# Kernel tuning notes

Measured on AMD Instinct MI355X. Metric: run time of the kernel, lower is better.

## Reference

```python
import jax, jax.numpy as jnp
import numpy as np
import math

N, T, IN = 2048, 128, 64
H = 256           # hidden_dim
NH, HD = 2, 128   # num_heads, head_dim (NH*HD == H)
C = 30            # rows of R
OUT = 1           # output_dim


def setup_inputs() -> dict:
    key = jax.random.key(0)
    ks = jax.random.split(key, 24)
    s = lambda k, shape, sc: (jax.random.normal(k, shape, dtype=jnp.float32) * sc)
    g = 1.0 / math.sqrt(H)
    d = {}
    d['x'] = s(ks[0], (N, T, IN), 1.0)
    # GRU layer 0 (input IN -> H); gate order r,z,n as in torch
    d['W_ih0'] = s(ks[1], (3 * H, IN), g)
    d['W_hh0'] = s(ks[2], (3 * H, H), g)
    d['b_ih0'] = s(ks[3], (3 * H,), g)
    d['b_hh0'] = s(ks[4], (3 * H,), g)
    # GRU layer 1 (H -> H)
    d['W_ih1'] = s(ks[5], (3 * H, H), g)
    d['W_hh1'] = s(ks[6], (3 * H, H), g)
    d['b_ih1'] = s(ks[7], (3 * H,), g)
    d['b_hh1'] = s(ks[8], (3 * H,), g)
    # per-head Q/K/V linears, stacked over heads: [NH, H, HD] (+ bias [NH, HD])
    d['Wq'] = s(ks[9], (NH, H, HD), g)
    d['bq'] = s(ks[10], (NH, HD), g)
    d['Wk'] = s(ks[11], (NH, H, HD), g)
    d['bk'] = s(ks[12], (NH, HD), g)
    d['Wv'] = s(ks[13], (NH, H, HD), g)
    d['bv'] = s(ks[14], (NH, HD), g)
    # fixed random memory R [C, H]
    d['R'] = s(ks[15], (C, H), 1.0)
    # gate, mlp1, mlp2
    d['W_gate'] = s(ks[16], (1, H), g)
    d['b_gate'] = s(ks[17], (1,), g)
    d['W1'] = s(ks[18], (H, H), g)
    d['b1'] = s(ks[19], (H,), g)
    d['W2'] = s(ks[20], (OUT, H), g)
    d['b2'] = s(ks[21], (OUT,), g)
    return d


def _gru_layer(xs, Wih, Whh, bih, bhh):
    # xs: [N, T, D_in] -> [N, T, H]; PyTorch GRU equations, gate order r,z,n
    xW = jnp.einsum('nti,gi->ntg', xs, Wih) + bih  # [N,T,3H] precompute input path
    h0 = jnp.zeros((xs.shape[0], H), xs.dtype)

    def step(h, xt):
        gh = h @ Whh.T + bhh                      # [N,3H]
        r = jax.nn.sigmoid(xt[:, :H] + gh[:, :H])
        z = jax.nn.sigmoid(xt[:, H:2 * H] + gh[:, H:2 * H])
        n = jnp.tanh(xt[:, 2 * H:] + r * gh[:, 2 * H:])
        hn = (1.0 - z) * n + z * h
        return hn, hn

    _, ys = jax.lax.scan(step, h0, jnp.swapaxes(xW, 0, 1))
    return jnp.swapaxes(ys, 0, 1)


def _mha(q, k, v, Wq, bq, Wk, bk, Wv, bv):
    # q:[Lq,H] k,v:[Lk,H]; vectorized over heads (replaces the per-head Python loop)
    qh = jnp.einsum('ld,ndh->nlh', q, Wq) + bq[:, None, :]
    kh = jnp.einsum('ld,ndh->nlh', k, Wk) + bk[:, None, :]
    vh = jnp.einsum('ld,ndh->nlh', v, Wv) + bv[:, None, :]
    p = jax.nn.softmax(jnp.einsum('nqh,nkh->nqk', qh, kh) / math.sqrt(HD), axis=-1)
    o = jnp.einsum('nqk,nkh->nqh', p, vh)
    # concat heads along last dim, head order preserved
    return jnp.swapaxes(o, 0, 1).reshape(q.shape[0], NH * HD)


def reference(x, W_ih0, W_hh0, b_ih0, b_hh0, W_ih1, W_hh1, b_ih1, b_hh1,
              Wq, bq, Wk, bk, Wv, bv, R, W_gate, b_gate, W1, b1, W2, b2):
    out = _gru_layer(x, W_ih0, W_hh0, b_ih0, b_hh0)
    out = _gru_layer(out, W_ih1, W_hh1, b_ih1, b_hh1)
    S = out[:, -1, :]                               # [N, H]
    B = _mha(R, S, S, Wq, bq, Wk, bk, Wv, bv)       # [C, H]
    S_prime = _mha(S, B, B, Wq, bq, Wk, bk, Wv, bv) # [N, H]
    alpha = jax.nn.sigmoid(S @ W_gate.T + b_gate)   # [N,1], broadcasts like expand_as
    S_mix = alpha * S_prime + (1.0 - alpha) * S
    h = jax.nn.relu(S_mix @ W1.T + b1)              # dropout = identity (eval mode)
    S_mix = h + S_mix
    y = (S_mix @ W2.T + b2).reshape(-1)             # [N*OUT]
    return (y - y.mean()) / (y.std(ddof=1) + 1e-8)  # torch.std is unbiased (ddof=1)
```

## Files before the change

kernel.cpp:

```cpp
#include <hip/hip_runtime.h>
#include <hip/hip_bf16.h>


#define HH  256
#define TT  128
#define INP 64
#define KH  8

typedef float f32x4 __attribute__((ext_vector_type(4)));
typedef short bf16x8 __attribute__((ext_vector_type(8)));
typedef unsigned long long u64;

#define MFMA(A,B,C) __builtin_amdgcn_mfma_f32_16x16x32_bf16((A),(B),(C),0,0,0)

__device__ __forceinline__ float bf2f(unsigned short s) {
    unsigned u = ((unsigned)s) << 16;
    float f; __builtin_memcpy(&f, &u, 4); return f;
}
__device__ __forceinline__ unsigned short f2bf(float f) {
    unsigned u; __builtin_memcpy(&u, &f, 4);
    unsigned r = (u + 0x7FFFu + ((u >> 16) & 1u)) >> 16;
    return (unsigned short)r;
}

__device__ __forceinline__ float sigm(float x) {
    float t = __builtin_amdgcn_exp2f(x * -1.442695040889f);
    return __builtin_amdgcn_rcpf(1.f + t);
}
__device__ __forceinline__ float tanhfast(float x) {
    float xc = fminf(fmaxf(x, -15.f), 15.f);
    float t = __builtin_amdgcn_exp2f(xc * 2.885390081778f);
    return (t - 1.f) * __builtin_amdgcn_rcpf(t + 1.f);
}


__global__ void pack_w(const float* __restrict__ Whh, const float* __restrict__ Wih,
                       int Kin, int Kw, unsigned short* __restrict__ FBhi,
                       unsigned short* __restrict__ FBlo, int total)
{
    int idx = blockIdx.x * 256 + threadIdx.x;
    if (idx >= total) return;
    int n = idx / Kw, k = idx - n * Kw;
    float v = (k < 256) ? Whh[n * 256 + k] : Wih[n * Kin + (k - 256)];
    int dst = (n >> 4) * (Kw * 16) + (k >> 5) * 512 + ((k >> 3) & 3) * 128 + (n & 15) * 8 + (k & 7);
    unsigned short h = f2bf(v);
    FBhi[dst] = h;
    FBlo[dst] = f2bf(v - bf2f(h));
}

__global__ void pack_x(const float* __restrict__ x, unsigned short* __restrict__ FXhi)
{
    int idx = blockIdx.x * 256 + threadIdx.x;
    int k = idx & 63;
    int t = (idx >> 6) & 127;
    int m = idx >> 13;
    int dst = t * 131072 + (m >> 4) * 1024 + (k >> 5) * 512 + ((k >> 3) & 3) * 128 + (m & 15) * 8 + (k & 7);
    FXhi[dst] = f2bf(x[idx]);
}

template<int NKC, int STRIDE>
__device__ __forceinline__ void stage_Bs(const unsigned short* __restrict__ Bhi,
                                         const unsigned short* __restrict__ Blo,
                                         short* __restrict__ sB, int ntb, int tid)
{
    const int Kw16 = NKC * 512;
#pragma unroll 1
    for (int t = tid; t < 3 * NKC * 64; t += STRIDE) {
        const int g = t / (NKC * 64);
        const int r = t - g * (NKC * 64);
        *(bf16x8*)(sB + g * Kw16 + r * 8) =
            *(const bf16x8*)(Bhi + (g * 16 + ntb) * Kw16 + r * 8);
        *(bf16x8*)(sB + 3 * Kw16 + g * Kw16 + r * 8) =
            *(const bf16x8*)(Blo + (g * 16 + ntb) * Kw16 + r * 8);
    }
}

template<int NKC, bool LAY>
__device__ __forceinline__ void gru_core(
    const unsigned short* Ah_h, const unsigned short* Al_h,
    const unsigned short* Ah_x, const unsigned short* Al_x,
    const short* __restrict__ sB, int mt0, int lane,
    f32x4 (&ar)[2], f32x4 (&az)[2], f32x4 (&anh)[2], f32x4 (&anx)[2])
{
    const int Kw16 = NKC * 512;
    const int xs = LAY ? 4096 : 1024;
    const int lo8 = lane * 8;
    const short* sH = sB + lo8;
    const short* sL = sB + 3 * Kw16 + lo8;

    bf16x8 A[4][2][2];
    bf16x8 B[3][3][2];

    auto ldA = [&](int kc, bf16x8 (&Ax)[2][2]) {
        if (kc < KH) {
#pragma unroll
            for (int mt = 0; mt < 2; ++mt) {
                Ax[mt][0] = *(const bf16x8*)(Ah_h + (mt0 + mt) * 4096 + kc * 512 + lo8);
                Ax[mt][1] = *(const bf16x8*)(Al_h + (mt0 + mt) * 4096 + kc * 512 + lo8);
            }
        } else {
#pragma unroll
            for (int mt = 0; mt < 2; ++mt) {
                Ax[mt][0] = *(const bf16x8*)(Ah_x + (mt0 + mt) * xs + (kc - KH) * 512 + lo8);
                if (LAY)
                    Ax[mt][1] = *(const bf16x8*)(Al_x + (mt0 + mt) * xs + (kc - KH) * 512 + lo8);
            }
        }
    };
    auto ldB = [&](int kc, bf16x8 (&Bx)[3][2]) {
#pragma unroll
        for (int g = 0; g < 3; ++g) {
            Bx[g][0] = *(const bf16x8*)(sH + g * Kw16 + kc * 512);
            Bx[g][1] = *(const bf16x8*)(sL + g * Kw16 + kc * 512);
        }
    };

    ldA(0, A[0]);
    if (NKC > 1) ldA(1, A[1]);
    if (NKC > 2) ldA(2, A[2]);
    ldB(0, B[0]);
    if (NKC > 1) ldB(1, B[1]);
#pragma unroll
    for (int kc = 0; kc < NKC; ++kc) {
        if (kc + 3 < NKC) ldA(kc + 3, A[(kc + 3) & 3]);
        if (kc + 2 < NKC) ldB(kc + 2, B[(kc + 2) % 3]);
        const bool hp = (kc < KH);
        const bool a3 = LAY || hp;
        bf16x8 (&cA)[2][2] = A[kc & 3];
        bf16x8 (&cB)[3][2] = B[kc % 3];
#pragma unroll
        for (int mt = 0; mt < 2; ++mt) {
            ar[mt] = MFMA(cA[mt][0], cB[0][0], ar[mt]);
            ar[mt] = MFMA(cA[mt][0], cB[0][1], ar[mt]);
            if (a3) ar[mt] = MFMA(cA[mt][1], cB[0][0], ar[mt]);
            az[mt] = MFMA(cA[mt][0], cB[1][0], az[mt]);
            az[mt] = MFMA(cA[mt][0], cB[1][1], az[mt]);
            if (a3) az[mt] = MFMA(cA[mt][1], cB[1][0], az[mt]);
            if (hp) {
                anh[mt] = MFMA(cA[mt][0], cB[2][0], anh[mt]);
                anh[mt] = MFMA(cA[mt][0], cB[2][1], anh[mt]);
                if (a3) anh[mt] = MFMA(cA[mt][1], cB[2][0], anh[mt]);
            } else {
                anx[mt] = MFMA(cA[mt][0], cB[2][0], anx[mt]);
                anx[mt] = MFMA(cA[mt][0], cB[2][1], anx[mt]);
                if (a3) anx[mt] = MFMA(cA[mt][1], cB[2][0], anx[mt]);
            }
        }
    }
}

__device__ __forceinline__ void xcd_bar(unsigned* cnt, unsigned need)
{
    __syncthreads();
    if (threadIdx.x == 0) {
        __hip_atomic_fetch_add(cnt, 1u, __ATOMIC_RELAXED, __HIP_MEMORY_SCOPE_AGENT);
        while (__hip_atomic_load(cnt, __ATOMIC_RELAXED, __HIP_MEMORY_SCOPE_AGENT) < need)
            __builtin_amdgcn_s_sleep(1);
    }
    __syncthreads();
    asm volatile("buffer_inv\n\ts_waitcnt vmcnt(0)" ::: "memory");
}

__global__ __launch_bounds__(512, 2) void gru_scan(
    unsigned short* H0hiA, unsigned short* H0loA,
    unsigned short* H0hiB, unsigned short* H0loB,
    unsigned short* H1hiA, unsigned short* H1loA,
    unsigned short* H1hiB, unsigned short* H1loB,
    const unsigned short* __restrict__ FXhi,
    const unsigned short* __restrict__ FB0hi, const unsigned short* __restrict__ FB0lo,
    const unsigned short* __restrict__ FB1hi, const unsigned short* __restrict__ FB1lo,
    const float* __restrict__ bih0, const float* __restrict__ bhh0,
    const float* __restrict__ bih1, const float* __restrict__ bhh1,
    float* __restrict__ S1f, unsigned* bar, int* xslot)
{
    const int tid = threadIdx.x;
    int xcc;
    asm volatile("s_getreg_b32 %0, hwreg(HW_REG_XCC_ID)" : "=s"(xcc));
    xcc &= 7;
    __shared__ int sSlot;
    if (tid == 0) sSlot = atomicAdd(&xslot[xcc], 1) & 31;
    __syncthreads();
    const int slot = sSlot;
    const int mb2 = slot >> 4;
    const int cb = slot & 15;
    const int w = tid >> 6, lane = tid & 63;
    const int lay = w >> 2, wl = w & 3;
    const int l15 = lane & 15, q = lane >> 4;
    const int mt0 = xcc * 16 + mb2 * 8 + wl * 2;
    const int ntb = cb;
    unsigned* cnt = bar + (xcc * 2 + mb2) * 32;

    __shared__ __align__(16) short sB[79872];
    short* sB1 = sB;
    short* sB0 = sB + 49152;
    stage_Bs<16, 512>(FB1hi, FB1lo, sB1, cb, tid);
    stage_Bs<10, 512>(FB0hi, FB0lo, sB0, cb, tid);
    __syncthreads();

    const float* bih = lay ? bih1 : bih0;
    const float* bhh = lay ? bhh1 : bhh0;
    const int c = (ntb << 4) + l15;
    const float brb = bih[c] + bhh[c];
    const float bzb = bih[256 + c] + bhh[256 + c];
    const float bni = bih[512 + c];
    const float bnh = bhh[512 + c];
    const int cfr = (c >> 5) * 512 + ((c >> 3) & 3) * 128 + (c & 7);

    float hreg[2][4];
#pragma unroll
    for (int mt = 0; mt < 2; ++mt)
#pragma unroll
        for (int rg = 0; rg < 4; ++rg) hreg[mt][rg] = 0.f;

    for (int i = 0; i <= TT; ++i) {
        const int p = i & 1;
        const unsigned short* H0r_hi = p ? H0hiB : H0hiA;
        const unsigned short* H0r_lo = p ? H0loB : H0loA;
        unsigned short*       H0w_hi = p ? H0hiA : H0hiB;
        unsigned short*       H0w_lo = p ? H0loA : H0loB;
        const unsigned short* H1r_hi = p ? H1hiB : H1hiA;
        const unsigned short* H1r_lo = p ? H1loB : H1loA;
        unsigned short*       H1w_hi = p ? H1hiA : H1hiB;
        unsigned short*       H1w_lo = p ? H1loA : H1loB;

        const bool active = lay ? (i >= 1) : (i < TT);
        if (active) {
            f32x4 ar[2], az[2], anh[2], anx[2];
#pragma unroll
            for (int j = 0; j < 2; ++j) {
                ar[j] = (f32x4){0.f,0.f,0.f,0.f}; az[j] = (f32x4){0.f,0.f,0.f,0.f};
                anh[j] = (f32x4){0.f,0.f,0.f,0.f}; anx[j] = (f32x4){0.f,0.f,0.f,0.f};
            }
            if (lay) {
                gru_core<16, true>(H1r_hi, H1r_lo, H0r_hi, H0r_lo, sB1,
                                   mt0, lane, ar, az, anh, anx);
            } else {
                gru_core<10, false>(H0r_hi, H0r_lo, FXhi + i * 131072,
                                    (const unsigned short*)0, sB0,
                                    mt0, lane, ar, az, anh, anx);
            }

            unsigned short* Whi = lay ? H1w_hi : H0w_hi;
            unsigned short* Wlo = lay ? H1w_lo : H0w_lo;

#pragma unroll
            for (int mt = 0; mt < 2; ++mt) {
                const int mtg = mt0 + mt;
                const int fbase = mtg * 4096 + cfr;
#pragma unroll
                for (int rg = 0; rg < 4; ++rg) {
                    const int mi = q * 4 + rg;
                    const int fidx = fbase + mi * 8;
                    const float rr = sigm(ar[mt][rg] + brb);
                    const float zz = sigm(az[mt][rg] + bzb);
                    const float nn = tanhfast(anx[mt][rg] + bni + rr * (anh[mt][rg] + bnh));
                    const float hn = (1.f - zz) * nn + zz * hreg[mt][rg];
                    const unsigned short hb = f2bf(hn);
                    const unsigned short lb = f2bf(hn - bf2f(hb));
                    Whi[fidx] = hb;
                    Wlo[fidx] = lb;
                    hreg[mt][rg] = bf2f(hb) + bf2f(lb);
                    if (lay && i == TT) S1f[(mtg * 16 + mi) * 256 + c] = hn;
                }
            }
        }
        if (i < TT) xcd_bar(cnt, 16u * (unsigned)(i + 1));
    }
}


__global__ __launch_bounds__(256) void proj_gemm(const float* __restrict__ S,
    const float* __restrict__ Wk, const float* __restrict__ bk,
    const float* __restrict__ Wv, const float* __restrict__ bv,
    const float* __restrict__ Wq, const float* __restrict__ bq,
    float* __restrict__ ok, float* __restrict__ ov, float* __restrict__ oq)
{
    __shared__ float sT[256][65];
    const int bid = blockIdx.x;
    const int p = bid >> 6;
    const int h = (bid >> 5) & 1;
    const int l0 = (bid & 31) * 64;
    const int tid = threadIdx.x;
    const float* W = (p == 0) ? Wk : ((p == 1) ? Wv : Wq);
    const float* b = (p == 0) ? bk : ((p == 1) ? bv : bq);
    float* o = (p == 0) ? ok : ((p == 1) ? ov : oq);

    for (int e = tid; e < 64 * 256; e += 256) {
        int k = e & 255, l = e >> 8;
        sT[k][l] = S[(l0 + l) * 256 + k];
    }
    __syncthreads();

    const int dg = tid & 15, lg = tid >> 4;
    const int d0 = dg * 8;
    const float* Wp = W + h * 32768 + d0;
    float acc[4][8];
#pragma unroll
    for (int i = 0; i < 4; ++i)
#pragma unroll
        for (int j = 0; j < 8; ++j) acc[i][j] = 0.f;

    for (int k = 0; k < 256; ++k) {
        f32x4 sv = *(const f32x4*)&sT[k][lg * 4];
        f32x4 w0 = *(const f32x4*)(Wp + k * 128);
        f32x4 w1 = *(const f32x4*)(Wp + k * 128 + 4);
#pragma unroll
        for (int i = 0; i < 4; ++i) {
#pragma unroll
            for (int j = 0; j < 4; ++j) {
                acc[i][j]     += sv[i] * w0[j];
                acc[i][4 + j] += sv[i] * w1[j];
            }
        }
    }
#pragma unroll
    for (int i = 0; i < 4; ++i) {
        float* op = o + (h * 2048 + l0 + lg * 4 + i) * 128 + d0;
#pragma unroll
        for (int j = 0; j < 8; ++j) op[j] = acc[i][j] + b[h * 128 + d0 + j];
    }
}

__global__ void proj3_kernel(const float* __restrict__ A, int M,
    const float* __restrict__ Wk, const float* __restrict__ bk,
    const float* __restrict__ Wv, const float* __restrict__ bv,
    float* __restrict__ ok, float* __restrict__ ov)
{
    int idx = blockIdx.x * 256 + threadIdx.x;
    if (idx >= 2 * 2 * M * 128) return;
    int d = idx & 127;
    int rest = idx >> 7;
    int l = rest % M;
    int ph = rest / M;
    int h = ph & 1, p = ph >> 1;
    const float* W = (p == 0) ? Wk : Wv;
    const float* b = (p == 0) ? bk : bv;
    float* o = (p == 0) ? ok : ov;
    float accv = b[h * 128 + d];
    const float* a = A + l * 256;
    const float* wp = W + h * (256 * 128) + d;
    for (int j = 0; j < 256; ++j) accv += a[j] * wp[j * 128];
    o[(h * M + l) * 128 + d] = accv;
}

__global__ void projR_kernel(const float* __restrict__ R,
    const float* __restrict__ Wq, const float* __restrict__ bq,
    float* __restrict__ oq)
{
    int idx = blockIdx.x * 256 + threadIdx.x;
    if (idx >= 2 * 30 * 128) return;
    int d = idx & 127;
    int rest = idx >> 7;
    int l = rest % 30;
    int h = rest / 30;
    float a = bq[h * 128 + d];
    const float* r = R + l * 256;
    const float* wp = Wq + h * 32768 + d;
    for (int j = 0; j < 256; ++j) a += r[j] * wp[j * 128];
    oq[(h * 30 + l) * 128 + d] = a;
}

__global__ void scores1_kernel(const float* __restrict__ qhR, const float* __restrict__ kh,
                               float* __restrict__ s1)
{
    int idx = blockIdx.x * 256 + threadIdx.x;
    if (idx >= 2 * 30 * 2048) return;
    int k = idx & 2047;
    int rest = idx >> 11;
    int i = rest % 30;
    int h = rest / 30;
    const f32x4* qp = (const f32x4*)(qhR + (h * 30 + i) * 128);
    const f32x4* kp = (const f32x4*)(kh + (h * 2048 + k) * 128);
    float acc = 0.f;
    for (int dd = 0; dd < 32; ++dd) {
        f32x4 a = qp[dd], b = kp[dd];
        acc += a[0] * b[0] + a[1] * b[1] + a[2] * b[2] + a[3] * b[3];
    }
    s1[idx] = acc * 0.08838834764831845f;
}

__global__ void softmax1_kernel(float* __restrict__ s1)
{
    __shared__ float red[256];
    float* p = s1 + blockIdx.x * 2048;
    int tid = threadIdx.x;
    float mx = -1e30f;
    for (int k = tid; k < 2048; k += 256) mx = fmaxf(mx, p[k]);
    red[tid] = mx; __syncthreads();
    for (int s = 128; s > 0; s >>= 1) { if (tid < s) red[tid] = fmaxf(red[tid], red[tid + s]); __syncthreads(); }
    mx = red[0]; __syncthreads();
    float sum = 0.f;
    for (int k = tid; k < 2048; k += 256) { float e = expf(p[k] - mx); p[k] = e; sum += e; }
    red[tid] = sum; __syncthreads();
    for (int s = 128; s > 0; s >>= 1) { if (tid < s) red[tid] += red[tid + s]; __syncthreads(); }
    float inv = 1.f / red[0];
    for (int k = tid; k < 2048; k += 256) p[k] *= inv;
}

__global__ void o1_kernel(const float* __restrict__ p1, const float* __restrict__ vh,
                          float* __restrict__ Bm)
{
    int bid = blockIdx.x;
    int row = bid >> 4;
    int ks = bid & 15;
    int h = row / 30;
    int i = row % 30;
    int d = threadIdx.x;
    const float* pp = p1 + row * 2048 + ks * 128;
    const float* vp = vh + (h * 2048 + ks * 128) * 128 + d;
    float acc = 0.f;
    for (int k = 0; k < 128; ++k) acc += pp[k] * vp[k * 128];
    atomicAdd(&Bm[i * 256 + h * 128 + d], acc);
}

__global__ __launch_bounds__(256) void attn2_kernel(
    const float* __restrict__ qh2, const float* __restrict__ kh2, const float* __restrict__ vh2,
    const float* __restrict__ S, const float* __restrict__ Wg,
    const float* __restrict__ bg, float* __restrict__ Smix)
{
    __shared__ float ks[2 * 30 * 129];
    __shared__ float qred[256];
    __shared__ float ps[64];
    int l = blockIdx.x;
    int tid = threadIdx.x;
    for (int idx = tid; idx < 2 * 30 * 128; idx += 256) {
        int hh = idx / 3840; int rem = idx - hh * 3840;
        int j = rem >> 7; int d = rem & 127;
        ks[(hh * 30 + j) * 129 + d] = kh2[idx];
    }
    int h = tid >> 7, d = tid & 127;
    qred[tid] = qh2[(h * 2048 + l) * 128 + d];
    __syncthreads();
    int w = tid >> 6, lane = tid & 63;
    if (w < 2 && lane < 32) {
        float sc = -1e30f;
        if (lane < 30) {
            const float* qp = qred + w * 128;
            float a = 0.f;
            for (int dd = 0; dd < 128; ++dd) a += qp[dd] * ks[(w * 30 + lane) * 129 + dd];
            sc = a * 0.08838834764831845f;
        }
        float mx = sc;
        for (int m = 16; m > 0; m >>= 1) mx = fmaxf(mx, __shfl_xor(mx, m, 32));
        float e = (lane < 30) ? expf(sc - mx) : 0.f;
        float sm = e;
        for (int m = 16; m > 0; m >>= 1) sm += __shfl_xor(sm, m, 32);
        ps[w * 32 + lane] = e / sm;
    }
    __syncthreads();
    float o = 0.f;
    const float* vp = vh2 + h * 3840 + d;
    for (int j = 0; j < 30; ++j) o += ps[h * 32 + j] * vp[j * 128];
    float sl = S[l * 256 + tid];
    qred[tid] = sl * Wg[tid];
    __syncthreads();
    for (int s = 128; s > 0; s >>= 1) { if (tid < s) qred[tid] += qred[tid + s]; __syncthreads(); }
    float alpha = 1.f / (1.f + expf(-(qred[0] + bg[0])));
    Smix[l * 256 + tid] = alpha * o + (1.f - alpha) * sl;
}

__global__ void w1t_kernel(const float* __restrict__ W1, float* __restrict__ W1T)
{
    int idx = blockIdx.x * 256 + threadIdx.x;
    int j = idx & 255, c = idx >> 8;
    W1T[j * 256 + c] = W1[c * 256 + j];
}

__global__ void mlp_kernel(const float* __restrict__ Smix, const float* __restrict__ W1T,
                           const float* __restrict__ b1, float* __restrict__ S2)
{
    int idx = blockIdx.x * 256 + threadIdx.x;
    int c = idx & 255; int l = idx >> 8;
    const float* a = Smix + l * 256;
    float acc = b1[c];
    for (int j = 0; j < 256; ++j) acc += a[j] * W1T[j * 256 + c];
    float v = fmaxf(acc, 0.f);
    S2[idx] = v + a[c];
}

__global__ void y_kernel(const float* __restrict__ S2, const float* __restrict__ W2,
                         const float* __restrict__ b2, float* __restrict__ y)
{
    __shared__ float red[256];
    int l = blockIdx.x; int tid = threadIdx.x;
    red[tid] = S2[l * 256 + tid] * W2[tid];
    __syncthreads();
    for (int s = 128; s > 0; s >>= 1) { if (tid < s) red[tid] += red[tid + s]; __syncthreads(); }
    if (tid == 0) y[l] = red[0] + b2[0];
}

__global__ void norm_kernel(const float* __restrict__ y, float* __restrict__ out)
{
    __shared__ float r1[1024], r2[1024];
    int tid = threadIdx.x;
    float s1v = 0.f, s2v = 0.f;
    for (int idx = tid; idx < 2048; idx += 1024) { float v = y[idx]; s1v += v; s2v += v * v; }
    r1[tid] = s1v; r2[tid] = s2v; __syncthreads();
    for (int s = 512; s > 0; s >>= 1) {
        if (tid < s) { r1[tid] += r1[tid + s]; r2[tid] += r2[tid + s]; }
        __syncthreads();
    }
    float mean = r1[0] / 2048.f;
    float var = fmaxf((r2[0] - 2048.f * mean * mean) / 2047.f, 0.f);
    float inv = 1.f / (sqrtf(var) + 1e-8f);
    for (int idx = tid; idx < 2048; idx += 1024)
        out[idx] = (y[idx] - mean) * inv;
}

extern "C" void kernel_launch(void* const* d_in, const int* in_sizes, int n_in,
                              void* d_out, int out_size, void* d_ws, size_t ws_size,
                              hipStream_t stream)
{
    const float* x    = (const float*)d_in[0];
    const float* Wih0 = (const float*)d_in[1];
    const float* Whh0 = (const float*)d_in[2];
    const float* bih0 = (const float*)d_in[3];
    const float* bhh0 = (const float*)d_in[4];
    const float* Wih1 = (const float*)d_in[5];
    const float* Whh1 = (const float*)d_in[6];
    const float* bih1 = (const float*)d_in[7];
    const float* bhh1 = (const float*)d_in[8];
    const float* Wq   = (const float*)d_in[9];
    const float* bq   = (const float*)d_in[10];
    const float* Wk   = (const float*)d_in[11];
    const float* bk   = (const float*)d_in[12];
    const float* Wv   = (const float*)d_in[13];
    const float* bv   = (const float*)d_in[14];
    const float* R    = (const float*)d_in[15];
    const float* Wg   = (const float*)d_in[16];
    const float* bg   = (const float*)d_in[17];
    const float* W1   = (const float*)d_in[18];
    const float* b1   = (const float*)d_in[19];
    const float* W2   = (const float*)d_in[20];
    const float* b2   = (const float*)d_in[21];

    float* ws = (float*)d_ws;
    size_t off = 0;
    auto alloc_f = [&](size_t n) { float* p = ws + off; off += n; return p; };
    float* S1f  = alloc_f(524288);
    float* kh   = alloc_f(524288);
    float* vh   = alloc_f(524288);
    float* qh2  = alloc_f(524288);
    float* qhR  = alloc_f(7680);
    float* s1   = alloc_f(122880);
    float* Bm   = alloc_f(7680);
    float* kh2  = alloc_f(7680);
    float* vh2  = alloc_f(7680);
    float* Smix = alloc_f(524288);
    float* S2   = alloc_f(524288);
    float* yv   = alloc_f(2048);
    float* W1T  = alloc_f(65536);
    unsigned short* us = (unsigned short*)(ws + off);
    size_t uoff = 0;
    auto alloc_u = [&](size_t n) { unsigned short* p = us + uoff; uoff += n; return p; };
    unsigned short* H0hi[2] = { alloc_u(524288), alloc_u(524288) };
    unsigned short* H0lo[2] = { alloc_u(524288), alloc_u(524288) };
    unsigned short* H1hi[2] = { alloc_u(524288), alloc_u(524288) };
    unsigned short* H1lo[2] = { alloc_u(524288), alloc_u(524288) };
    unsigned short* FB0hi = alloc_u(245760);
    unsigned short* FB0lo = alloc_u(245760);
    unsigned short* FB1hi = alloc_u(393216);
    unsigned short* FB1lo = alloc_u(393216);
    unsigned short* FXhi  = alloc_u(16777216);
    unsigned* barp = (unsigned*)alloc_u(1024);
    int* xslotp = (int*)alloc_u(16);

    pack_w<<<960, 256, 0, stream>>>(Whh0, Wih0, 64, 320, FB0hi, FB0lo, 245760);
    pack_w<<<1536, 256, 0, stream>>>(Whh1, Wih1, 256, 512, FB1hi, FB1lo, 393216);
    pack_x<<<65536, 256, 0, stream>>>(x, FXhi);
    (void)hipMemsetAsync(H0hi[0], 0, 1048576, stream);
    (void)hipMemsetAsync(H0lo[0], 0, 1048576, stream);
    (void)hipMemsetAsync(H1hi[1], 0, 1048576, stream);
    (void)hipMemsetAsync(H1lo[1], 0, 1048576, stream);
    (void)hipMemsetAsync(Bm, 0, 30720, stream);
    (void)hipMemsetAsync(barp, 0, 2048, stream);
    (void)hipMemsetAsync(xslotp, 0, 32, stream);

    gru_scan<<<256, 512, 0, stream>>>(
        H0hi[0], H0lo[0], H0hi[1], H0lo[1],
        H1hi[0], H1lo[0], H1hi[1], H1lo[1],
        FXhi, FB0hi, FB0lo, FB1hi, FB1lo,
        bih0, bhh0, bih1, bhh1, S1f, barp, xslotp);

    proj_gemm<<<192, 256, 0, stream>>>(S1f, Wk, bk, Wv, bv, Wq, bq, kh, vh, qh2);
    projR_kernel<<<30, 256, 0, stream>>>(R, Wq, bq, qhR);
    scores1_kernel<<<480, 256, 0, stream>>>(qhR, kh, s1);
    softmax1_kernel<<<60, 256, 0, stream>>>(s1);
    o1_kernel<<<960, 128, 0, stream>>>(s1, vh, Bm);
    proj3_kernel<<<60, 256, 0, stream>>>(Bm, 30, Wk, bk, Wv, bv, kh2, vh2);
    attn2_kernel<<<2048, 256, 0, stream>>>(qh2, kh2, vh2, S1f, Wg, bg, Smix);
    w1t_kernel<<<256, 256, 0, stream>>>(W1, W1T);
    mlp_kernel<<<2048, 256, 0, stream>>>(Smix, W1T, b1, S2);
    y_kernel<<<2048, 256, 0, stream>>>(S2, W2, b2, yv);
    norm_kernel<<<1, 1024, 0, stream>>>(yv, (float*)d_out);
}
```

Before: 1.279 ms.

## Split GRU step K-reduction across wave pairs with global-scratch partial exchange

Doubles the GRU scan block to 1024 threads: each pair of waves splits the K chunks of the recurrent MFMA reduction in half. The partner's partial accumulators for one m-tile are exchanged through a global scratch buffer after a block barrier, and each wave then runs the gate nonlinearity for one m-tile. The aim is to shorten the per-timestep critical path by adding parallelism and latency hiding. The cost is an extra __syncthreads plus global scratch traffic every step, and the deeper A/B register prefetch pipeline is reduced to shrink register use.

```diff
diff --git a/kernel.cpp b/kernel.cpp
--- a/kernel.cpp
+++ b/kernel.cpp
@@ -75,7 +75,7 @@
     }
 }
 
-template<int NKC, bool LAY>
+template<int K0, int K1, int NKC, bool LAY>
 __device__ __forceinline__ void gru_core(
     const unsigned short* Ah_h, const unsigned short* Al_h,
     const unsigned short* Ah_x, const unsigned short* Al_x,
@@ -88,8 +88,7 @@
     const short* sH = sB + lo8;
     const short* sL = sB + 3 * Kw16 + lo8;
 
-    bf16x8 A[4][2][2];
-    bf16x8 B[3][3][2];
+    bf16x8 A[2][2][2];
 
     auto ldA = [&](int kc, bf16x8 (&Ax)[2][2]) {
         if (kc < KH) {
@@ -107,27 +106,20 @@
             }
         }
     };
-    auto ldB = [&](int kc, bf16x8 (&Bx)[3][2]) {
+
+    ldA(K0, A[0]);
+#pragma unroll
+    for (int kc = K0; kc < K1; ++kc) {
+        if (kc + 1 < K1) ldA(kc + 1, A[(kc - K0 + 1) & 1]);
+        bf16x8 cB[3][2];
 #pragma unroll
         for (int g = 0; g < 3; ++g) {
-            Bx[g][0] = *(const bf16x8*)(sH + g * Kw16 + kc * 512);
-            Bx[g][1] = *(const bf16x8*)(sL + g * Kw16 + kc * 512);
+            cB[g][0] = *(const bf16x8*)(sH + g * Kw16 + kc * 512);
+            cB[g][1] = *(const bf16x8*)(sL + g * Kw16 + kc * 512);
         }
-    };
-
-    ldA(0, A[0]);
-    if (NKC > 1) ldA(1, A[1]);
-    if (NKC > 2) ldA(2, A[2]);
-    ldB(0, B[0]);
-    if (NKC > 1) ldB(1, B[1]);
-#pragma unroll
-    for (int kc = 0; kc < NKC; ++kc) {
-        if (kc + 3 < NKC) ldA(kc + 3, A[(kc + 3) & 3]);
-        if (kc + 2 < NKC) ldB(kc + 2, B[(kc + 2) % 3]);
         const bool hp = (kc < KH);
         const bool a3 = LAY || hp;
-        bf16x8 (&cA)[2][2] = A[kc & 3];
-        bf16x8 (&cB)[3][2] = B[kc % 3];
+        bf16x8 (&cA)[2][2] = A[(kc - K0) & 1];
 #pragma unroll
         for (int mt = 0; mt < 2; ++mt) {
             ar[mt] = MFMA(cA[mt][0], cB[0][0], ar[mt]);
@@ -161,7 +153,7 @@
     asm volatile("buffer_inv\n\ts_waitcnt vmcnt(0)" ::: "memory");
 }
 
-__global__ __launch_bounds__(512, 2) void gru_scan(
+__global__ __launch_bounds__(1024) void gru_scan(
     unsigned short* H0hiA, unsigned short* H0loA,
     unsigned short* H0hiB, unsigned short* H0loB,
     unsigned short* H1hiA, unsigned short* H1loA,
@@ -171,7 +163,7 @@
     const unsigned short* __restrict__ FB1hi, const unsigned short* __restrict__ FB1lo,
     const float* __restrict__ bih0, const float* __restrict__ bhh0,
     const float* __restrict__ bih1, const float* __restrict__ bhh1,
-    float* __restrict__ S1f, unsigned* bar, int* xslot)
+    float* __restrict__ S1f, unsigned* bar, int* xslot, float* __restrict__ scr)
 {
     const int tid = threadIdx.x;
     int xcc;
@@ -184,17 +176,22 @@
     const int mb2 = slot >> 4;
     const int cb = slot & 15;
     const int w = tid >> 6, lane = tid & 63;
-    const int lay = w >> 2, wl = w & 3;
+    const int lay = w >> 3;
+    const int w7 = w & 7;
+    const int wl = w7 >> 1, ks = w7 & 1;
     const int l15 = lane & 15, q = lane >> 4;
     const int mt0 = xcc * 16 + mb2 * 8 + wl * 2;
+    const int my_mt = mt0 + ks;
     const int ntb = cb;
     unsigned* cnt = bar + (xcc * 2 + mb2) * 32;
+    float* myslot = scr + ((((int)blockIdx.x << 4) + w) * 64 + lane) * 16;
+    float* paslot = scr + ((((int)blockIdx.x << 4) + (w ^ 1)) * 64 + lane) * 16;
 
     __shared__ __align__(16) short sB[79872];
     short* sB1 = sB;
     short* sB0 = sB + 49152;
-    stage_Bs<16, 512>(FB1hi, FB1lo, sB1, cb, tid);
-    stage_Bs<10, 512>(FB0hi, FB0lo, sB0, cb, tid);
+    stage_Bs<16, 1024>(FB1hi, FB1lo, sB1, cb, tid);
+    stage_Bs<10, 1024>(FB0hi, FB0lo, sB0, cb, tid);
     __syncthreads();
 
     const float* bih = lay ? bih1 : bih0;
@@ -206,11 +203,7 @@
     const float bnh = bhh[512 + c];
     const int cfr = (c >> 5) * 512 + ((c >> 3) & 3) * 128 + (c & 7);
 
-    float hreg[2][4];
-#pragma unroll
-    for (int mt = 0; mt < 2; ++mt)
-#pragma unroll
-        for (int rg = 0; rg < 4; ++rg) hreg[mt][rg] = 0.f;
+    float hreg[4] = {0.f, 0.f, 0.f, 0.f};
 
     for (int i = 0; i <= TT; ++i) {
         const int p = i & 1;
@@ -224,44 +217,69 @@
         unsigned short*       H1w_lo = p ? H1loA : H1loB;
 
         const bool active = lay ? (i >= 1) : (i < TT);
+        f32x4 ar[2], az[2], anh[2], anx[2];
         if (active) {
-            f32x4 ar[2], az[2], anh[2], anx[2];
 #pragma unroll
             for (int j = 0; j < 2; ++j) {
                 ar[j] = (f32x4){0.f,0.f,0.f,0.f}; az[j] = (f32x4){0.f,0.f,0.f,0.f};
                 anh[j] = (f32x4){0.f,0.f,0.f,0.f}; anx[j] = (f32x4){0.f,0.f,0.f,0.f};
             }
             if (lay) {
-                gru_core<16, true>(H1r_hi, H1r_lo, H0r_hi, H0r_lo, sB1,
-                                   mt0, lane, ar, az, anh, anx);
+                if (ks == 0)
+                    gru_core<0, 8, 16, true>(H1r_hi, H1r_lo, H0r_hi, H0r_lo, sB1,
+                                             mt0, lane, ar, az, anh, anx);
+                else
+                    gru_core<8, 16, 16, true>(H1r_hi, H1r_lo, H0r_hi, H0r_lo, sB1,
+                                              mt0, lane, ar, az, anh, anx);
             } else {
-                gru_core<10, false>(H0r_hi, H0r_lo, FXhi + i * 131072,
-                                    (const unsigned short*)0, sB0,
-                                    mt0, lane, ar, az, anh, anx);
-            }
+                if (ks == 0)
+                    gru_core<0, 5, 10, false>(H0r_hi, H0r_lo, FXhi + i * 131072,
+                                              (const unsigned short*)0, sB0,
+                                              mt0, lane, ar, az, anh, anx);
+                else
+                    gru_core<5, 10, 10, false>(H0r_hi, H0r_lo, FXhi + i * 131072,
+                                               (const unsigned short*)0, sB0,
+                                               mt0, lane, ar, az, anh, anx);
+            }
+            if (ks == 0) {
+                *(f32x4*)(myslot)      = ar[1];
+                *(f32x4*)(myslot + 4)  = az[1];
+                *(f32x4*)(myslot + 8)  = anh[1];
+                *(f32x4*)(myslot + 12) = anx[1];
+            } else {
+                *(f32x4*)(myslot)      = ar[0];
+                *(f32x4*)(myslot + 4)  = az[0];
+                *(f32x4*)(myslot + 8)  = anh[0];
+                *(f32x4*)(myslot + 12) = anx[0];
+            }
+        }
+        __syncthreads();
+        if (active) {
+            f32x4 pr  = *(const f32x4*)(paslot);
+            f32x4 pz  = *(const f32x4*)(paslot + 4);
+            f32x4 pnh = *(const f32x4*)(paslot + 8);
+            f32x4 pnx = *(const f32x4*)(paslot + 12);
+            f32x4 car, caz, cnh, cnx;
+            if (ks == 0) { car = ar[0] + pr; caz = az[0] + pz; cnh = anh[0] + pnh; cnx = anx[0] + pnx; }
+            else         { car = ar[1] + pr; caz = az[1] + pz; cnh = anh[1] + pnh; cnx = anx[1] + pnx; }
 
             unsigned short* Whi = lay ? H1w_hi : H0w_hi;
             unsigned short* Wlo = lay ? H1w_lo : H0w_lo;
-
-#pragma unroll
-            for (int mt = 0; mt < 2; ++mt) {
-                const int mtg = mt0 + mt;
-                const int fbase = mtg * 4096 + cfr;
-#pragma unroll
-                for (int rg = 0; rg < 4; ++rg) {
-                    const int mi = q * 4 + rg;
-                    const int fidx = fbase + mi * 8;
-                    const float rr = sigm(ar[mt][rg] + brb);
-                    const float zz = sigm(az[mt][rg] + bzb);
-                    const float nn = tanhfast(anx[mt][rg] + bni + rr * (anh[mt][rg] + bnh));
-                    const float hn = (1.f - zz) * nn + zz * hreg[mt][rg];
-                    const unsigned short hb = f2bf(hn);
-                    const unsigned short lb = f2bf(hn - bf2f(hb));
-                    Whi[fidx] = hb;
-                    Wlo[fidx] = lb;
-                    hreg[mt][rg] = bf2f(hb) + bf2f(lb);
-                    if (lay && i == TT) S1f[(mtg * 16 + mi) * 256 + c] = hn;
-                }
+            const int fbase = my_mt * 4096 + cfr;
+#pragma unroll
+            for (int rg = 0; rg < 4; ++rg) {
+                const int mi = q * 4 + rg;
+                const int fidx = fbase + mi * 8;
+                const float rr = sigm(car[rg] + brb);
+                const float zz = sigm(caz[rg] + bzb);
+                const float nn = tanhfast(cnx[rg] + bni + rr * (cnh[rg] + bnh));
+                const float hn = (1.f - zz) * nn + zz * hreg[rg];
+                const unsigned short hb = f2bf(hn);
+                const unsigned short lb = f2bf(hn - bf2f(hb));
+                Whi[fidx] = hb;
+                Wlo[fidx] = lb;
+                hreg[rg] = bf2f(hb) + bf2f(lb);
+                if (lay && i == TT) S1f[(my_mt * 16 + mi) * 256 + c] = hn;
             }
         }
         if (i < TT) xcd_bar(cnt, 16u * (unsigned)(i + 1));
@@ -550,6 +568,7 @@
     float* S2   = alloc_f(524288);
     float* yv   = alloc_f(2048);
     float* W1T  = alloc_f(65536);
+    float* pscr = alloc_f(4194304);
     unsigned short* us = (unsigned short*)(ws + off);
     size_t uoff = 0;
     auto alloc_u = [&](size_t n) { unsigned short* p = us + uoff; uoff += n; return p; };
@@ -576,11 +595,11 @@
     (void)hipMemsetAsync(barp, 0, 2048, stream);
     (void)hipMemsetAsync(xslotp, 0, 32, stream);
 
-    gru_scan<<<256, 512, 0, stream>>>(
+    gru_scan<<<256, 1024, 0, stream>>>(
         H0hi[0], H0lo[0], H0hi[1], H0lo[1],
         H1hi[0], H1lo[0], H1hi[1], H1lo[1],
         FXhi, FB0hi, FB0lo, FB1hi, FB1lo,
-        bih0, bhh0, bih1, bhh1, S1f, barp, xslotp);
+        bih0, bhh0, bih1, bhh1, S1f, barp, xslotp, pscr);
 
     proj_gemm<<<192, 256, 0, stream>>>(S1f, Wk, bk, Wv, bv, Wq, bq, kh, vh, qh2);
     projR_kernel<<<30, 256, 0, stream>>>(R, Wq, bq, qhR);
```

Result: slower. 1.930 ms (+50.8%).

## Switch GRU scan MFMAs to fp16 single-weight split and double block count

Applied to the files above, without the earlier changes.

Replaces the bf16 hi/lo weight splitting with a single fp16 weight copy (keeping the hidden state as an fp16 hi/lo pair). This cuts the MFMA count per k-chunk from three to two and halves the LDS footprint for weights. Each wave now handles one M-tile instead of two, and the launch grows to 512 blocks at 4 blocks per CU, with more barrier groups per XCD. The trade-off is fp16 weight precision and range, plus more blocks taking part in each per-step cross-block barrier.

```diff
diff --git a/kernel.cpp b/kernel.cpp
--- a/kernel.cpp
+++ b/kernel.cpp
@@ -9,18 +9,17 @@
 
 typedef float f32x4 __attribute__((ext_vector_type(4)));
 typedef short bf16x8 __attribute__((ext_vector_type(8)));
+typedef _Float16 f16x8 __attribute__((ext_vector_type(8)));
 typedef unsigned long long u64;
 
-#define MFMA(A,B,C) __builtin_amdgcn_mfma_f32_16x16x32_bf16((A),(B),(C),0,0,0)
-
-__device__ __forceinline__ float bf2f(unsigned short s) {
-    unsigned u = ((unsigned)s) << 16;
-    float f; __builtin_memcpy(&f, &u, 4); return f;
-}
-__device__ __forceinline__ unsigned short f2bf(float f) {
-    unsigned u; __builtin_memcpy(&u, &f, 4);
-    unsigned r = (u + 0x7FFFu + ((u >> 16) & 1u)) >> 16;
-    return (unsigned short)r;
+#define MFMA16(A,B,C) __builtin_amdgcn_mfma_f32_16x16x32_f16((A),(B),(C),0,0,0)
+
+__device__ __forceinline__ unsigned short f2h(float f) {
+    _Float16 h = (_Float16)f;
+    unsigned short u; __builtin_memcpy(&u, &h, 2); return u;
+}
+__device__ __forceinline__ float h2f(unsigned short u) {
+    _Float16 h; __builtin_memcpy(&h, &u, 2); return (float)h;
 }
 
 __device__ __forceinline__ float sigm(float x) {
@@ -35,32 +34,28 @@
 
 
 __global__ void pack_w(const float* __restrict__ Whh, const float* __restrict__ Wih,
-                       int Kin, int Kw, unsigned short* __restrict__ FBhi,
-                       unsigned short* __restrict__ FBlo, int total)
+                       int Kin, int Kw, unsigned short* __restrict__ FBh, int total)
 {
     int idx = blockIdx.x * 256 + threadIdx.x;
     if (idx >= total) return;
     int n = idx / Kw, k = idx - n * Kw;
     float v = (k < 256) ? Whh[n * 256 + k] : Wih[n * Kin + (k - 256)];
     int dst = (n >> 4) * (Kw * 16) + (k >> 5) * 512 + ((k >> 3) & 3) * 128 + (n & 15) * 8 + (k & 7);
-    unsigned short h = f2bf(v);
-    FBhi[dst] = h;
-    FBlo[dst] = f2bf(v - bf2f(h));
-}
-
-__global__ void pack_x(const float* __restrict__ x, unsigned short* __restrict__ FXhi)
+    FBh[dst] = f2h(v);
+}
+
+__global__ void pack_x(const float* __restrict__ x, unsigned short* __restrict__ FXh)
 {
     int idx = blockIdx.x * 256 + threadIdx.x;
     int k = idx & 63;
     int t = (idx >> 6) & 127;
     int m = idx >> 13;
     int dst = t * 131072 + (m >> 4) * 1024 + (k >> 5) * 512 + ((k >> 3) & 3) * 128 + (m & 15) * 8 + (k & 7);
-    FXhi[dst] = f2bf(x[idx]);
+    FXh[dst] = f2h(x[idx]);
 }
 
 template<int NKC, int STRIDE>
-__device__ __forceinline__ void stage_Bs(const unsigned short* __restrict__ Bhi,
-                                         const unsigned short* __restrict__ Blo,
+__device__ __forceinline__ void stage_Bs(const unsigned short* __restrict__ Bh,
                                          short* __restrict__ sB, int ntb, int tid)
 {
     const int Kw16 = NKC * 512;
@@ -69,9 +64,7 @@
         const int g = t / (NKC * 64);
         const int r = t - g * (NKC * 64);
         *(bf16x8*)(sB + g * Kw16 + r * 8) =
-            *(const bf16x8*)(Bhi + (g * 16 + ntb) * Kw16 + r * 8);
-        *(bf16x8*)(sB + 3 * Kw16 + g * Kw16 + r * 8) =
-            *(const bf16x8*)(Blo + (g * 16 + ntb) * Kw16 + r * 8);
+            *(const bf16x8*)(Bh + (g * 16 + ntb) * Kw16 + r * 8);
     }
 }
 
@@ -79,72 +72,55 @@
 __device__ __forceinline__ void gru_core(
     const unsigned short* Ah_h, const unsigned short* Al_h,
     const unsigned short* Ah_x, const unsigned short* Al_x,
-    const short* __restrict__ sB, int mt0, int lane,
-    f32x4 (&ar)[2], f32x4 (&az)[2], f32x4 (&anh)[2], f32x4 (&anx)[2])
+    const short* __restrict__ sB, int mt, int lane,
+    f32x4& ar, f32x4& az, f32x4& anh, f32x4& anx)
 {
     const int Kw16 = NKC * 512;
     const int xs = LAY ? 4096 : 1024;
     const int lo8 = lane * 8;
-    const short* sH = sB + lo8;
-    const short* sL = sB + 3 * Kw16 + lo8;
-
-    bf16x8 A[4][2][2];
-    bf16x8 B[3][3][2];
-
-    auto ldA = [&](int kc, bf16x8 (&Ax)[2][2]) {
+    const short* sBl = sB + lo8;
+
+    f16x8 A[4][2];
+    f16x8 B[2][3];
+
+    auto ldA = [&](int kc, f16x8 (&Ax)[2]) {
         if (kc < KH) {
-#pragma unroll
-            for (int mt = 0; mt < 2; ++mt) {
-                Ax[mt][0] = *(const bf16x8*)(Ah_h + (mt0 + mt) * 4096 + kc * 512 + lo8);
-                Ax[mt][1] = *(const bf16x8*)(Al_h + (mt0 + mt) * 4096 + kc * 512 + lo8);
-            }
+            Ax[0] = *(const f16x8*)(Ah_h + mt * 4096 + kc * 512 + lo8);
+            Ax[1] = *(const f16x8*)(Al_h + mt * 4096 + kc * 512 + lo8);
         } else {
-#pragma unroll
-            for (int mt = 0; mt < 2; ++mt) {
-                Ax[mt][0] = *(const bf16x8*)(Ah_x + (mt0 + mt) * xs + (kc - KH) * 512 + lo8);
-                if (LAY)
-                    Ax[mt][1] = *(const bf16x8*)(Al_x + (mt0 + mt) * xs + (kc - KH) * 512 + lo8);
-            }
+            Ax[0] = *(const f16x8*)(Ah_x + mt * xs + (kc - KH) * 512 + lo8);
+            if (LAY)
+                Ax[1] = *(const f16x8*)(Al_x + mt * xs + (kc - KH) * 512 + lo8);
         }
     };
-    auto ldB = [&](int kc, bf16x8 (&Bx)[3][2]) {
-#pragma unroll
-        for (int g = 0; g < 3; ++g) {
-            Bx[g][0] = *(const bf16x8*)(sH + g * Kw16 + kc * 512);
-            Bx[g][1] = *(const bf16x8*)(sL + g * Kw16 + kc * 512);
-        }
+    auto ldB = [&](int kc, f16x8 (&Bx)[3]) {
+#pragma unroll
+        for (int g = 0; g < 3; ++g)
+            Bx[g] = *(const f16x8*)(sBl + g * Kw16 + kc * 512);
     };
 
     ldA(0, A[0]);
     if (NKC > 1) ldA(1, A[1]);
     if (NKC > 2) ldA(2, A[2]);
     ldB(0, B[0]);
-    if (NKC > 1) ldB(1, B[1]);
 #pragma unroll
     for (int kc = 0; kc < NKC; ++kc) {
         if (kc + 3 < NKC) ldA(kc + 3, A[(kc + 3) & 3]);
-        if (kc + 2 < NKC) ldB(kc + 2, B[(kc + 2) % 3]);
+        if (kc + 1 < NKC) ldB(kc + 1, B[(kc + 1) & 1]);
         const bool hp = (kc < KH);
-        const bool a3 = LAY || hp;
-        bf16x8 (&cA)[2][2] = A[kc & 3];
-        bf16x8 (&cB)[3][2] = B[kc % 3];
-#pragma unroll
-        for (int mt = 0; mt < 2; ++mt) {
-            ar[mt] = MFMA(cA[mt][0], cB[0][0], ar[mt]);
-            ar[mt] = MFMA(cA[mt][0], cB[0][1], ar[mt]);
-            if (a3) ar[mt] = MFMA(cA[mt][1], cB[0][0], ar[mt]);
-            az[mt] = MFMA(cA[mt][0], cB[1][0], az[mt]);
-            az[mt] = MFMA(cA[mt][0], cB[1][1], az[mt]);
-            if (a3) az[mt] = MFMA(cA[mt][1], cB[1][0], az[mt]);
-            if (hp) {
-                anh[mt] = MFMA(cA[mt][0], cB[2][0], anh[mt]);
-                anh[mt] = MFMA(cA[mt][0], cB[2][1], anh[mt]);
-                if (a3) anh[mt] = MFMA(cA[mt][1], cB[2][0], anh[mt]);
-            } else {
-                anx[mt] = MFMA(cA[mt][0], cB[2][0], anx[mt]);
-                anx[mt] = MFMA(cA[mt][0], cB[2][1], anx[mt]);
-                if (a3) anx[mt] = MFMA(cA[mt][1], cB[2][0], anx[mt]);
-            }
+        const bool a2 = LAY || hp;
+        f16x8 (&cA)[2] = A[kc & 3];
+        f16x8 (&cB)[3] = B[kc & 1];
+        ar = MFMA16(cA[0], cB[0], ar);
+        if (a2) ar = MFMA16(cA[1], cB[0], ar);
+        az = MFMA16(cA[0], cB[1], az);
+        if (a2) az = MFMA16(cA[1], cB[1], az);
+        if (hp) {
+            anh = MFMA16(cA[0], cB[2], anh);
+            if (a2) anh = MFMA16(cA[1], cB[2], anh);
+        } else {
+            anx = MFMA16(cA[0], cB[2], anx);
+            if (a2) anx = MFMA16(cA[1], cB[2], anx);
         }
     }
 }
@@ -161,14 +137,13 @@
     asm volatile("buffer_inv\n\ts_waitcnt vmcnt(0)" ::: "memory");
 }
 
-__global__ __launch_bounds__(512, 2) void gru_scan(
+__global__ __launch_bounds__(512, 4) void gru_scan(
     unsigned short* H0hiA, unsigned short* H0loA,
     unsigned short* H0hiB, unsigned short* H0loB,
     unsigned short* H1hiA, unsigned short* H1loA,
     unsigned short* H1hiB, unsigned short* H1loB,
-    const unsigned short* __restrict__ FXhi,
-    const unsigned short* __restrict__ FB0hi, const unsigned short* __restrict__ FB0lo,
-    const unsigned short* __restrict__ FB1hi, const unsigned short* __restrict__ FB1lo,
+    const unsigned short* __restrict__ FXh,
+    const unsigned short* __restrict__ FB0h, const unsigned short* __restrict__ FB1h,
     const float* __restrict__ bih0, const float* __restrict__ bhh0,
     const float* __restrict__ bih1, const float* __restrict__ bhh1,
     float* __restrict__ S1f, unsigned* bar, int* xslot)
@@ -178,23 +153,23 @@
     asm volatile("s_getreg_b32 %0, hwreg(HW_REG_XCC_ID)" : "=s"(xcc));
     xcc &= 7;
     __shared__ int sSlot;
-    if (tid == 0) sSlot = atomicAdd(&xslot[xcc], 1) & 31;
+    if (tid == 0) sSlot = atomicAdd(&xslot[xcc], 1) & 63;
     __syncthreads();
     const int slot = sSlot;
-    const int mb2 = slot >> 4;
+    const int mb4 = slot >> 4;
     const int cb = slot & 15;
     const int w = tid >> 6, lane = tid & 63;
     const int lay = w >> 2, wl = w & 3;
     const int l15 = lane & 15, q = lane >> 4;
-    const int mt0 = xcc * 16 + mb2 * 8 + wl * 2;
+    const int mt = xcc * 16 + mb4 * 4 + wl;
     const int ntb = cb;
-    unsigned* cnt = bar + (xcc * 2 + mb2) * 32;
-
-    __shared__ __align__(16) short sB[79872];
+    unsigned* cnt = bar + (xcc * 4 + mb4) * 32;
+
+    __shared__ __align__(16) short sB[39936];
     short* sB1 = sB;
-    short* sB0 = sB + 49152;
-    stage_Bs<16, 512>(FB1hi, FB1lo, sB1, cb, tid);
-    stage_Bs<10, 512>(FB0hi, FB0lo, sB0, cb, tid);
+    short* sB0 = sB + 24576;
+    stage_Bs<16, 512>(FB1h, sB1, cb, tid);
+    stage_Bs<10, 512>(FB0h, sB0, cb, tid);
     __syncthreads();
 
     const float* bih = lay ? bih1 : bih0;
@@ -206,11 +181,7 @@
     const float bnh = bhh[512 + c];
     const int cfr = (c >> 5) * 512 + ((c >> 3) & 3) * 128 + (c & 7);
 
-    float hreg[2][4];
-#pragma unroll
-    for (int mt = 0; mt < 2; ++mt)
-#pragma unroll
-        for (int rg = 0; rg < 4; ++rg) hreg[mt][rg] = 0.f;
+    float hreg[4] = {0.f, 0.f, 0.f, 0.f};
 
     for (int i = 0; i <= TT; ++i) {
         const int p = i & 1;
@@ -225,43 +196,34 @@
 
         const bool active = lay ? (i >= 1) : (i < TT);
         if (active) {
-            f32x4 ar[2], az[2], anh[2], anx[2];
-#pragma unroll
-            for (int j = 0; j < 2; ++j) {
-                ar[j] = (f32x4){0.f,0.f,0.f,0.f}; az[j] = (f32x4){0.f,0.f,0.f,0.f};
-                anh[j] = (f32x4){0.f,0.f,0.f,0.f}; anx[j] = (f32x4){0.f,0.f,0.f,0.f};
-            }
+            f32x4 ar = {0.f,0.f,0.f,0.f}, az = {0.f,0.f,0.f,0.f};
+            f32x4 anh = {0.f,0.f,0.f,0.f}, anx = {0.f,0.f,0.f,0.f};
             if (lay) {
                 gru_core<16, true>(H1r_hi, H1r_lo, H0r_hi, H0r_lo, sB1,
-                                   mt0, lane, ar, az, anh, anx);
+                                   mt, lane, ar, az, anh, anx);
             } else {
-                gru_core<10, false>(H0r_hi, H0r_lo, FXhi + i * 131072,
+                gru_core<10, false>(H0r_hi, H0r_lo, FXh + i * 131072,
                                     (const unsigned short*)0, sB0,
-                                    mt0, lane, ar, az, anh, anx);
+                                    mt, lane, ar, az, anh, anx);
             }
 
             unsigned short* Whi = lay ? H1w_hi : H0w_hi;
             unsigned short* Wlo = lay ? H1w_lo : H0w_lo;
-
-#pragma unroll
-            for (int mt = 0; mt < 2; ++mt) {
-                const int mtg = mt0 + mt;
-                const int fbase = mtg * 4096 + cfr;
-#pragma unroll
-                for (int rg = 0; rg < 4; ++rg) {
-                    const int mi = q * 4 + rg;
-                    const int fidx = fbase + mi * 8;
-                    const float rr = sigm(ar[mt][rg] + brb);
-                    const float zz = sigm(az[mt][rg] + bzb);
-                    const float nn = tanhfast(anx[mt][rg] + bni + rr * (anh[mt][rg] + bnh));
-                    const float hn = (1.f - zz) * nn + zz * hreg[mt][rg];
-                    const unsigned short hb = f2bf(hn);
-                    const unsigned short lb = f2bf(hn - bf2f(hb));
-                    Whi[fidx] = hb;
-                    Wlo[fidx] = lb;
-                    hreg[mt][rg] = bf2f(hb) + bf2f(lb);
-                    if (lay && i == TT) S1f[(mtg * 16 + mi) * 256 + c] = hn;
-                }
+            const int fbase = mt * 4096 + cfr;
+#pragma unroll
+            for (int rg = 0; rg < 4; ++rg) {
+                const int mi = q * 4 + rg;
+                const int fidx = fbase + mi * 8;
+                const float rr = sigm(ar[rg] + brb);
+                const float zz = sigm(az[rg] + bzb);
+                const float nn = tanhfast(anx[rg] + bni + rr * (anh[rg] + bnh));
+                const float hn = (1.f - zz) * nn + zz * hreg[rg];
+                const unsigned short hb = f2h(hn);
+                const unsigned short lb = f2h(hn - h2f(hb));
+                Whi[fidx] = hb;
+                Wlo[fidx] = lb;
+                hreg[rg] = h2f(hb) + h2f(lb);
+                if (lay && i == TT) S1f[(mt * 16 + mi) * 256 + c] = hn;
             }
         }
         if (i < TT) xcd_bar(cnt, 16u * (unsigned)(i + 1));
@@ -557,29 +519,27 @@
     unsigned short* H0lo[2] = { alloc_u(524288), alloc_u(524288) };
     unsigned short* H1hi[2] = { alloc_u(524288), alloc_u(524288) };
     unsigned short* H1lo[2] = { alloc_u(524288), alloc_u(524288) };
-    unsigned short* FB0hi = alloc_u(245760);
-    unsigned short* FB0lo = alloc_u(245760);
-    unsigned short* FB1hi = alloc_u(393216);
-    unsigned short* FB1lo = alloc_u(393216);
-    unsigned short* FXhi  = alloc_u(16777216);
-    unsigned* barp = (unsigned*)alloc_u(1024);
+    unsigned short* FB0h = alloc_u(245760);
+    unsigned short* FB1h = alloc_u(393216);
+    unsigned short* FXh  = alloc_u(16777216);
+    unsigned* barp = (unsigned*)alloc_u(2048);
     int* xslotp = (int*)alloc_u(16);
 
-    pack_w<<<960, 256, 0, stream>>>(Whh0, Wih0, 64, 320, FB0hi, FB0lo, 245760);
-    pack_w<<<1536, 256, 0, stream>>>(Whh1, Wih1, 256, 512, FB1hi, FB1lo, 393216);
-    pack_x<<<65536, 256, 0, stream>>>(x, FXhi);
+    pack_w<<<960, 256, 0, stream>>>(Whh0, Wih0, 64, 320, FB0h, 245760);
+    pack_w<<<1536, 256, 0, stream>>>(Whh1, Wih1, 256, 512, FB1h, 393216);
+    pack_x<<<65536, 256, 0, stream>>>(x, FXh);
     (void)hipMemsetAsync(H0hi[0], 0, 1048576, stream);
     (void)hipMemsetAsync(H0lo[0], 0, 1048576, stream);
     (void)hipMemsetAsync(H1hi[1], 0, 1048576, stream);
     (void)hipMemsetAsync(H1lo[1], 0, 1048576, stream);
     (void)hipMemsetAsync(Bm, 0, 30720, stream);
-    (void)hipMemsetAsync(barp, 0, 2048, stream);
+    (void)hipMemsetAsync(barp, 0, 4096, stream);
     (void)hipMemsetAsync(xslotp, 0, 32, stream);
 
-    gru_scan<<<256, 512, 0, stream>>>(
+    gru_scan<<<512, 512, 0, stream>>>(
         H0hi[0], H0lo[0], H0hi[1], H0lo[1],
         H1hi[0], H1lo[0], H1hi[1], H1lo[1],
-        FXhi, FB0hi, FB0lo, FB1hi, FB1lo,
+        FXh, FB0h, FB1h,
         bih0, bhh0, bih1, bhh1, S1f, barp, xslotp);
 
     proj_gemm<<<192, 256, 0, stream>>>(S1f, Wk, bk, Wv, bv, Wq, bq, kh, vh, qh2);
```

Result: slower. 1.687 ms (+31.8%).
